# Optimization experiments

Measured on AMD Instinct MI355X. Metric: run time of the kernel, lower is better.

The kernel has to match this reference:

```python
import jax, jax.numpy as jnp
import numpy as np

B, L, D_IN, H, FEAT, PROJ = 1024, 128, 130, 768, 49, 40


def setup_inputs() -> dict:
    key = jax.random.key(0)
    ks = jax.random.split(key, 16)
    s = 0.05
    return {
        "X": jax.random.normal(ks[0], (B, L, D_IN), dtype=jnp.float32),
        "Fe": jax.random.normal(ks[1], (B, FEAT), dtype=jnp.float32),
        # three attention heads densa1/2/3 stacked: [3, H, L]
        "W_att": jax.random.normal(ks[2], (3, H, L), dtype=jnp.float32) * s,
        "b_att": jax.random.normal(ks[3], (3, L), dtype=jnp.float32) * s,
        # LSTMCell(3*D_IN, H) params, PyTorch layout
        "W_ih": jax.random.normal(ks[4], (4 * H, 3 * D_IN), dtype=jnp.float32) * s,
        "W_hh": jax.random.normal(ks[5], (4 * H, H), dtype=jnp.float32) * s,
        "b_ih": jax.random.normal(ks[6], (4 * H,), dtype=jnp.float32) * s,
        "b_hh": jax.random.normal(ks[7], (4 * H,), dtype=jnp.float32) * s,
        # Dense1: Linear(H, FEAT)
        "W_d1": jax.random.normal(ks[8], (FEAT, H), dtype=jnp.float32) * s,
        "b_d1": jax.random.normal(ks[9], (FEAT,), dtype=jnp.float32) * s,
        # AttFeat R: Linear(FEAT, PROJ); A: Linear(PROJ, 1, bias=False)
        "W_r": jax.random.normal(ks[10], (PROJ, FEAT), dtype=jnp.float32) * s,
        "b_r": jax.random.normal(ks[11], (PROJ,), dtype=jnp.float32) * s,
        "W_a": jax.random.normal(ks[12], (1, PROJ), dtype=jnp.float32) * s,
        # Dense2: Linear(PROJ, 2)
        "W_d2": jax.random.normal(ks[13], (2, PROJ), dtype=jnp.float32) * s,
        "b_d2": jax.random.normal(ks[14], (2,), dtype=jnp.float32) * s,
    }


def reference(X, Fe, W_att, b_att, W_ih, W_hh, b_ih, b_hh, W_d1, b_d1, W_r, b_r, W_a, W_d2, b_d2):
    b = X.shape[0]

    def step(carry, _):
        h, c = carry
        # three softmax attention distributions over the sequence: [b, 3, L]
        logits = jnp.einsum('bh,khl->bkl', h, W_att) + b_att
        alp = jax.nn.softmax(logits, axis=-1)
        # weighted sums over seq -> concat of v1,v2,v3: [b, 3*D_IN]
        v = jnp.einsum('bkl,bld->bkd', alp, X).reshape(b, -1)
        # PyTorch LSTMCell update
        gates = v @ W_ih.T + b_ih + h @ W_hh.T + b_hh
        i, f, g, o = jnp.split(gates, 4, axis=-1)
        c_new = jax.nn.sigmoid(f) * c + jax.nn.sigmoid(i) * jnp.tanh(g)
        h_new = jax.nn.sigmoid(o) * jnp.tanh(c_new)
        return (h_new, c_new), h_new

    h0 = jnp.zeros((b, H), dtype=X.dtype)
    c0 = jnp.zeros((b, H), dtype=X.dtype)
    _, hs = jax.lax.scan(step, (h0, c0), None, length=L)  # [L, b, H]
    out = jnp.transpose(hs, (1, 0, 2))                    # [b, L, H]

    # MaxLayer: max-pool over the sequence dim
    x = jnp.max(out, axis=1)                              # [b, H]

    # Dense1 + ReLU
    y = jax.nn.relu(x @ W_d1.T + b_d1)                    # [b, FEAT]

    # AttFeat over [y, Fe]
    r1 = jax.nn.leaky_relu(y @ W_r.T + b_r)               # [b, PROJ]
    r2 = jax.nn.leaky_relu(Fe @ W_r.T + b_r)
    a1 = jnp.tanh(r1) @ W_a.T                             # [b, 1]
    a2 = jnp.tanh(r2) @ W_a.T
    a = jax.nn.softmax(jnp.concatenate([a1, a2], axis=-1), axis=-1)  # [b, 2]
    s = jax.nn.relu(a[:, 0:1] * r1 + a[:, 1:2] * r2)      # [b, PROJ]

    # Dense2 (squeeze is a no-op for b > 1)
    return s @ W_d2.T + b_d2                              # [b, 2]
```

## Files before the change

kernel.cpp:

```cpp
#include <hip/hip_runtime.h>
#include <stdint.h>


#define B_SZ   1024
#define LSEQ   128
#define DIN    130
#define HDIM   768
#define NFEAT  49
#define NPROJ  40
#define KPAD   1216
#define VOFF   416
#define NGATE  3072
#define KT_G   19
#define XELEM  (LSEQ * DIN)
#define GBUF   20480

typedef unsigned short u16;
typedef __attribute__((ext_vector_type(8))) short short8;
typedef __attribute__((ext_vector_type(4))) float f32x4;

__device__ __forceinline__ u16 f2bf(float f) {
  unsigned int u = __float_as_uint(f);
  u += 0x7FFFu + ((u >> 16) & 1u);
  return (u16)(u >> 16);
}
__device__ __forceinline__ float bf2f(u16 b) {
  return __uint_as_float(((unsigned int)b) << 16);
}
__device__ __forceinline__ float frcp(float x) {
  return __builtin_amdgcn_rcpf(x);
}
__device__ __forceinline__ float ftanh(float x) {
  return 1.f - 2.f * frcp(1.f + __expf(2.f * x));
}
__device__ __forceinline__ float fsigm(float x) {
  return frcp(1.f + __expf(-x));
}
__device__ __forceinline__ void gload16(const void* g, void* l) {
  __builtin_amdgcn_global_load_lds(
      (__attribute__((address_space(1))) const void*)g,
      (__attribute__((address_space(3))) void*)l, 16, 0, 0);
}

__global__ __launch_bounds__(256, 4) void gemm_logits_k(
    const u16* __restrict__ Ah,
    const u16* __restrict__ Bh, float* __restrict__ Cp)
{
  __shared__ __align__(16) u16 sAh[32 * 40];
  __shared__ __align__(16) u16 sBh[64 * 40];

  const int tid = threadIdx.x, lane = tid & 63, wid = tid >> 6;
  const int wm = (wid & 1) * 16, wn = (wid >> 1) * 32;
  const int lm = lane & 15, quad = lane >> 4;
  const int bm = blockIdx.x * 32, bn = blockIdx.y * 64;
  const int kh = blockIdx.z;
  const int kbase = kh * 384;
  float* __restrict__ C = Cp + (size_t)kh * B_SZ * 384;

  const bool aload = tid < 128;
  const int ar = tid >> 2, ac = (tid & 3) * 8;
  const size_t a_off = (size_t)(bm + ar) * KPAD + kbase + ac;
  const size_t b_off = (size_t)(bn + ar) * HDIM + kbase + ac;

  uint4 ph, pb;
  if (aload) ph = *(const uint4*)(Ah + a_off);
  pb = *(const uint4*)(Bh + b_off);

  f32x4 acc0 = {0.f, 0.f, 0.f, 0.f}, acc1 = {0.f, 0.f, 0.f, 0.f};

  for (int kt = 0; kt < 12; ++kt) {
    if (aload) *(uint4*)&sAh[ar * 40 + ac] = ph;
    *(uint4*)&sBh[ar * 40 + ac] = pb;
    __syncthreads();
    if (kt + 1 < 12) {
      const int k0 = (kt + 1) * 32;
      if (aload) ph = *(const uint4*)(Ah + a_off + k0);
      pb = *(const uint4*)(Bh + b_off + k0);
    }
    const short8 ah = *(const short8*)&sAh[(wm + lm) * 40 + quad * 8];
    const short8 b0 = *(const short8*)&sBh[(wn + lm) * 40 + quad * 8];
    const short8 b1 = *(const short8*)&sBh[(wn + 16 + lm) * 40 + quad * 8];
    acc0 = __builtin_amdgcn_mfma_f32_16x16x32_bf16(ah, b0, acc0, 0, 0, 0);
    acc1 = __builtin_amdgcn_mfma_f32_16x16x32_bf16(ah, b1, acc1, 0, 0, 0);
    __syncthreads();
  }

  const int col = bn + wn + lm;
  const int row0 = bm + wm + quad * 4;
#pragma unroll
  for (int r = 0; r < 4; ++r) {
    C[(size_t)(row0 + r) * 384 + col]      = acc0[r];
    C[(size_t)(row0 + r) * 384 + col + 16] = acc1[r];
  }
}

__global__ __launch_bounds__(256, 2) void gates_lstm(
    const u16* __restrict__ Ah,
    const u16* __restrict__ Wh,
    const float* __restrict__ bsum,
    float* __restrict__ cst, float* __restrict__ hmax,
    u16* __restrict__ out_h)
{
  __shared__ __align__(16) char smem[2 * GBUF];

  const int tid = threadIdx.x, lane = tid & 63, wid = tid >> 6;
  const int wm = (wid >> 1) * 32, wn = (wid & 1) * 48;
  const int lm = lane & 15, quad = lane >> 4;

  const int wg = blockIdx.x;
  const int vid = (wg & 7) * 64 + (wg >> 3);
  const int bm = (vid & 15) * 64;
  const int j0 = (vid >> 4) * 24;

  const u16* Asrc[2];
#pragma unroll
  for (int i = 0; i < 2; ++i) {
    const int r = i * 32 + wid * 8 + (lane >> 3);
    const int s = (lane & 7) ^ (r & 7);
    Asrc[i] = Ah + (size_t)(bm + r) * KPAD + (s << 3);
  }
  const u16* Bsrc[3];
#pragma unroll
  for (int i = 0; i < 3; ++i) {
    const int r = i * 32 + wid * 8 + (lane >> 3);
    const int s = (lane & 7) ^ (r & 7);
    const int nrow = (r / 24) * HDIM + j0 + (r % 24);
    Bsrc[i] = Wh + (size_t)nrow * KPAD + (s << 3);
  }

  int aoff[2], boff[3];
#pragma unroll
  for (int mi = 0; mi < 2; ++mi) {
    const int R = wm + mi * 16 + lm;
    aoff[mi] = R * 64 + ((quad ^ (R & 7)) << 3);
  }
#pragma unroll
  for (int ni = 0; ni < 3; ++ni) {
    const int R = wn + ni * 16 + lm;
    boff[ni] = R * 64 + ((quad ^ (R & 7)) << 3);
  }

  f32x4 acc[2][3];
#pragma unroll
  for (int mi = 0; mi < 2; ++mi)
#pragma unroll
    for (int ni = 0; ni < 3; ++ni) acc[mi][ni] = (f32x4){0.f, 0.f, 0.f, 0.f};

  auto stage = [&](int buf, int kt) {
    char* bb = smem + buf * GBUF;
    const int k0 = kt * 64;
#pragma unroll
    for (int i = 0; i < 2; ++i)
      gload16(Asrc[i] + k0, bb + ((i << 12) + (wid << 10)));
#pragma unroll
    for (int i = 0; i < 3; ++i)
      gload16(Bsrc[i] + k0, bb + 8192 + ((i << 12) + (wid << 10)));
  };

  stage(0, 0);
  __syncthreads();

  for (int kt = 0; kt < KT_G; ++kt) {
    if (kt + 1 < KT_G) stage((kt + 1) & 1, kt + 1);
    const u16* sA = (const u16*)(smem + (kt & 1) * GBUF);
    const u16* sB = sA + 4096;
#pragma unroll
    for (int kk = 0; kk < 2; ++kk) {
      const int kx = kk << 5;
      short8 af[2], bg[3];
#pragma unroll
      for (int mi = 0; mi < 2; ++mi)
        af[mi] = *(const short8*)(sA + (aoff[mi] ^ kx));
#pragma unroll
      for (int ni = 0; ni < 3; ++ni)
        bg[ni] = *(const short8*)(sB + (boff[ni] ^ kx));
#pragma unroll
      for (int mi = 0; mi < 2; ++mi)
#pragma unroll
        for (int ni = 0; ni < 3; ++ni)
          acc[mi][ni] = __builtin_amdgcn_mfma_f32_16x16x32_bf16(
              af[mi], bg[ni], acc[mi][ni], 0, 0, 0);
    }
    __syncthreads();
  }

  float* tile = (float*)smem;
#pragma unroll
  for (int mi = 0; mi < 2; ++mi)
#pragma unroll
    for (int ni = 0; ni < 3; ++ni) {
      const int c = wn + ni * 16 + lm;
#pragma unroll
      for (int r = 0; r < 4; ++r)
        tile[(wm + mi * 16 + quad * 4 + r) * 100 + c] = acc[mi][ni][r];
    }
  __syncthreads();

#pragma unroll
  for (int i = 0; i < 6; ++i) {
    const int lin = tid + 256 * i;
    const int row = lin / 24, jj = lin - row * 24;
    const int b = bm + row, j = j0 + jj;
    const float* tr = tile + row * 100;
    const float pi = tr[jj]      + bsum[j];
    const float pf = tr[24 + jj] + bsum[HDIM + j];
    const float pg = tr[48 + jj] + bsum[2 * HDIM + j];
    const float po = tr[72 + jj] + bsum[3 * HDIM + j];
    const float si = fsigm(pi);
    const float sf = fsigm(pf);
    const float so = fsigm(po);
    const size_t cidx = (size_t)b * HDIM + j;
    const float cn = sf * cst[cidx] + si * ftanh(pg);
    const float hn = so * ftanh(cn);
    cst[cidx] = cn;
    hmax[cidx] = fmaxf(hmax[cidx], hn);
    out_h[(size_t)b * KPAD + VOFF + j] = f2bf(hn);
  }
}

__global__ __launch_bounds__(512, 4) void softmax_v(
    const float* __restrict__ l0, const float* __restrict__ l1,
    const float* __restrict__ b_att,
    const u16* __restrict__ XT,
    u16* __restrict__ act)
{
  const int b = blockIdx.x;
  const int t = threadIdx.x;
  __shared__ __align__(16) u16 sXT[XELEM];
  __shared__ __align__(16) float s_alp[384];
  __shared__ float s_w[16];

  {
    const uint4* src = (const uint4*)(XT + (size_t)b * XELEM);
    uint4* dst = (uint4*)sXT;
#pragma unroll
    for (int rep = 0; rep < 4; ++rep) {
      const int i = t + rep * 512;
      const int d = i >> 4, blk = i & 15;
      dst[d * 16 + (blk ^ (d & 7))] = src[i];
    }
    if (t < 32) {
      const int i = 2048 + t;
      const int d = i >> 4, blk = i & 15;
      dst[d * 16 + (blk ^ (d & 7))] = src[i];
    }
  }

  const int lane = t & 63, wv = t >> 6, hw = wv & ~1;
  float x = -3.4e38f;
  if (t < 384)
    x = l0[(size_t)b * 384 + t] + l1[(size_t)b * 384 + t] + b_att[t];

  float m = x;
#pragma unroll
  for (int off = 32; off > 0; off >>= 1) m = fmaxf(m, __shfl_xor(m, off));
  if (lane == 0 && wv < 6) s_w[wv] = m;
  __syncthreads();

  float e = 0.f;
  if (t < 384) e = __expf(x - fmaxf(s_w[hw], s_w[hw | 1]));
  float sum = e;
#pragma unroll
  for (int off = 32; off > 0; off >>= 1) sum += __shfl_xor(sum, off);
  if (lane == 0 && wv < 6) s_w[8 + wv] = sum;
  __syncthreads();

  if (t < 384) {
    const float sk = s_w[8 + hw] + s_w[8 + (hw | 1)];
    s_alp[t] = e * frcp(sk);
  }
  __syncthreads();

  if (t < 390) {
    const int k = t / 130;
    const int d = t - k * 130;
    const uint4* xr = (const uint4*)sXT;
    const int dbase = d * 16, dsw = d & 7;
    const float* ab = s_alp + (k << 7);
    float acc = 0.f;
#pragma unroll
    for (int c = 0; c < 16; ++c) {
      const uint4 raw = xr[dbase + (c ^ dsw)];
      const float4 a0 = *(const float4*)(ab + (c << 3));
      const float4 a1 = *(const float4*)(ab + (c << 3) + 4);
      acc += a0.x * bf2f((u16)(raw.x & 0xffff));
      acc += a0.y * bf2f((u16)(raw.x >> 16));
      acc += a0.z * bf2f((u16)(raw.y & 0xffff));
      acc += a0.w * bf2f((u16)(raw.y >> 16));
      acc += a1.x * bf2f((u16)(raw.z & 0xffff));
      acc += a1.y * bf2f((u16)(raw.z >> 16));
      acc += a1.z * bf2f((u16)(raw.w & 0xffff));
      acc += a1.w * bf2f((u16)(raw.w >> 16));
    }
    act[(size_t)b * KPAD + t] = f2bf(acc);
  }
}

__global__ __launch_bounds__(64) void final_head(
    const float* __restrict__ hmax, const float* __restrict__ Fe,
    const float* __restrict__ W_d1, const float* __restrict__ b_d1,
    const float* __restrict__ W_r,  const float* __restrict__ b_r,
    const float* __restrict__ W_a,
    const float* __restrict__ W_d2, const float* __restrict__ b_d2,
    float* __restrict__ out)
{
  const int b = blockIdx.x;
  const int t = threadIdx.x;
  __shared__ float sx[HDIM];
  __shared__ float sy[NFEAT];
  __shared__ float sr1[NPROJ], sr2[NPROJ];
  __shared__ float sa[2];

  for (int i = t; i < HDIM; i += 64) sx[i] = hmax[(size_t)b * HDIM + i];
  __syncthreads();

  if (t < NFEAT) {
    float acc = b_d1[t];
    const float* w = W_d1 + (size_t)t * HDIM;
    for (int i = 0; i < HDIM; ++i) acc += sx[i] * w[i];
    sy[t] = fmaxf(acc, 0.f);
  }
  __syncthreads();

  if (t < NPROJ) {
    float a1 = b_r[t], a2 = b_r[t];
    const float* w  = W_r + (size_t)t * NFEAT;
    const float* fe = Fe + (size_t)b * NFEAT;
    for (int i = 0; i < NFEAT; ++i) { a1 += sy[i] * w[i]; a2 += fe[i] * w[i]; }
    sr1[t] = (a1 > 0.f) ? a1 : 0.01f * a1;
    sr2[t] = (a2 > 0.f) ? a2 : 0.01f * a2;
  }
  __syncthreads();

  if (t == 0) {
    float a1 = 0.f, a2 = 0.f;
    for (int p = 0; p < NPROJ; ++p) {
      a1 += tanhf(sr1[p]) * W_a[p];
      a2 += tanhf(sr2[p]) * W_a[p];
    }
    const float mx = fmaxf(a1, a2);
    const float e1 = expf(a1 - mx), e2 = expf(a2 - mx);
    sa[0] = e1 / (e1 + e2);
    sa[1] = e2 / (e1 + e2);
  }
  __syncthreads();

  if (t < 2) {
    float acc = b_d2[t];
    const float* w = W_d2 + (size_t)t * NPROJ;
    for (int p = 0; p < NPROJ; ++p) {
      float s = sa[0] * sr1[p] + sa[1] * sr2[p];
      s = fmaxf(s, 0.f);
      acc += s * w[p];
    }
    out[(size_t)b * 2 + t] = acc;
  }
}

__global__ __launch_bounds__(256) void pack_w(
    const float* __restrict__ W_ih, const float* __restrict__ W_hh,
    const float* __restrict__ b_ih, const float* __restrict__ b_hh,
    u16* __restrict__ hi, float* __restrict__ bsum)
{
  const int idx = blockIdx.x * 256 + threadIdx.x;
  if (idx >= NGATE * KPAD) return;
  const int n = idx / KPAD;
  const int k = idx - n * KPAD;
  float v = 0.f;
  if (k < 3 * DIN)                       v = W_ih[(size_t)n * (3 * DIN) + k];
  else if (k >= VOFF && k < VOFF + HDIM) v = W_hh[(size_t)n * HDIM + (k - VOFF)];
  hi[idx] = f2bf(v);
  if (k == 0) bsum[n] = b_ih[n] + b_hh[n];
}

__global__ __launch_bounds__(256) void pack_watt(
    const float* __restrict__ W_att,
    u16* __restrict__ hi)
{
  const int idx = blockIdx.x * 256 + threadIdx.x;
  if (idx >= 384 * HDIM) return;
  const int n = idx / HDIM;
  const int h = idx - n * HDIM;
  const int katt = n >> 7;
  const int l = n & 127;
  hi[idx] = f2bf(W_att[((size_t)katt * HDIM + h) * LSEQ + l]);
}

__global__ __launch_bounds__(256) void pack_xt(
    const float* __restrict__ X, u16* __restrict__ XT)
{
  const int b = blockIdx.x;
  const int t = threadIdx.x;
  __shared__ u16 sX[XELEM];
  const float* src = X + (size_t)b * XELEM;
  for (int i = t; i < XELEM; i += 256) sX[i] = f2bf(src[i]);
  __syncthreads();
  uint4* dst = (uint4*)(XT + (size_t)b * XELEM);
  for (int u = t; u < 2080; u += 256) {
    const int d = u >> 4, blk = u & 15;
    const int lb = blk * 8;
    ushort4 w0, w1;
    w0.x = sX[(lb + 0) * DIN + d]; w0.y = sX[(lb + 1) * DIN + d];
    w0.z = sX[(lb + 2) * DIN + d]; w0.w = sX[(lb + 3) * DIN + d];
    w1.x = sX[(lb + 4) * DIN + d]; w1.y = sX[(lb + 5) * DIN + d];
    w1.z = sX[(lb + 6) * DIN + d]; w1.w = sX[(lb + 7) * DIN + d];
    uint4 o;
    o.x = (unsigned)w0.x | ((unsigned)w0.y << 16);
    o.y = (unsigned)w0.z | ((unsigned)w0.w << 16);
    o.z = (unsigned)w1.x | ((unsigned)w1.y << 16);
    o.w = (unsigned)w1.z | ((unsigned)w1.w << 16);
    dst[u] = o;
  }
}

__global__ __launch_bounds__(256) void init_state(
    u16* __restrict__ a0, u16* __restrict__ a1,
    float* __restrict__ cst, float* __restrict__ hmax)
{
  const int idx = blockIdx.x * 256 + threadIdx.x;
  if (idx < B_SZ * KPAD) { a0[idx] = 0; a1[idx] = 0; }
  if (idx < B_SZ * HDIM) { cst[idx] = 0.f; hmax[idx] = -3.4e38f; }
}

extern "C" void kernel_launch(void* const* d_in, const int* in_sizes, int n_in,
                              void* d_out, int out_size, void* d_ws, size_t ws_size,
                              hipStream_t stream) {
  const float* X     = (const float*)d_in[0];
  const float* Fe    = (const float*)d_in[1];
  const float* W_att = (const float*)d_in[2];
  const float* b_att = (const float*)d_in[3];
  const float* W_ih  = (const float*)d_in[4];
  const float* W_hh  = (const float*)d_in[5];
  const float* b_ih  = (const float*)d_in[6];
  const float* b_hh  = (const float*)d_in[7];
  const float* W_d1  = (const float*)d_in[8];
  const float* b_d1  = (const float*)d_in[9];
  const float* W_r   = (const float*)d_in[10];
  const float* b_r   = (const float*)d_in[11];
  const float* W_a   = (const float*)d_in[12];
  const float* W_d2  = (const float*)d_in[13];
  const float* b_d2  = (const float*)d_in[14];
  float* out = (float*)d_out;

  char* base = (char*)d_ws;
  size_t off = 0;
  auto alloc = [&](size_t nbytes) -> void* {
    void* p = base + off;
    off = (off + nbytes + 255) & ~(size_t)255;
    return p;
  };
  u16* act0    = (u16*)alloc((size_t)B_SZ * KPAD * 2);
  u16* act1    = (u16*)alloc((size_t)B_SZ * KPAD * 2);
  u16* wcat    = (u16*)alloc((size_t)NGATE * KPAD * 2);
  u16* watt    = (u16*)alloc((size_t)384 * HDIM * 2);
  u16* xt16    = (u16*)alloc((size_t)B_SZ * XELEM * 2);
  float* bsum  = (float*)alloc((size_t)NGATE * 4);
  float* lpart = (float*)alloc((size_t)2 * B_SZ * 384 * 4);
  float* cst   = (float*)alloc((size_t)B_SZ * HDIM * 4);
  float* hmax  = (float*)alloc((size_t)B_SZ * HDIM * 4);

  pack_w<<<(NGATE * KPAD + 255) / 256, 256, 0, stream>>>(W_ih, W_hh, b_ih, b_hh, wcat, bsum);
  pack_watt<<<(384 * HDIM + 255) / 256, 256, 0, stream>>>(W_att, watt);
  pack_xt<<<B_SZ, 256, 0, stream>>>(X, xt16);
  init_state<<<(B_SZ * KPAD + 255) / 256, 256, 0, stream>>>(act0, act1, cst, hmax);

  float* l0 = lpart;
  float* l1 = lpart + (size_t)B_SZ * 384;

  gemm_logits_k<<<dim3(B_SZ / 32, 384 / 64, 2), 256, 0, stream>>>(act0 + VOFF, watt, lpart);
  softmax_v<<<B_SZ, 512, 0, stream>>>(l0, l1, b_att, xt16, act0);

  u16 *rd = act0, *wr = act1;
  for (int step = 0; step < LSEQ; ++step) {
    gates_lstm<<<dim3(512), 256, 0, stream>>>(rd, wcat, bsum, cst, hmax, wr);
    if (step + 1 < LSEQ) {
      gemm_logits_k<<<dim3(B_SZ / 32, 384 / 64, 2), 256, 0, stream>>>(wr + VOFF, watt, lpart);
      softmax_v<<<B_SZ, 512, 0, stream>>>(l0, l1, b_att, xt16, wr);
    }
    u16* tt = rd; rd = wr; wr = tt;
  }

  final_head<<<B_SZ, 64, 0, stream>>>(hmax, Fe, W_d1, b_d1, W_r, b_r, W_a, W_d2, b_d2, out);
}
```

Measured before the change: 4.356 ms.

## Enlarge gates_lstm tile to 128x96 with 512 threads and split waitcnt

The LSTM gate GEMM now runs 256 workgroups of 512 threads, each computing a 128-row by 96-gate-column tile instead of 64 rows. This halves how often the weight tiles are reloaded across workgroups and gives one larger block per CU. The shared-memory stage buffer grows to hold the bigger A tile. The full __syncthreads is replaced by per-wave s_waitcnt vmcnt counts plus s_barrier, so the next stage's loads can stay in flight while the current tile is computed. The cost is fewer, larger blocks with less latency hiding between blocks, and correctness now depends on the hand-counted outstanding loads per wave.

```diff
diff --git a/kernel.cpp b/kernel.cpp
--- a/kernel.cpp
+++ b/kernel.cpp
@@ -13,7 +13,7 @@
 #define NGATE  3072
 #define KT_G   19
 #define XELEM  (LSEQ * DIN)
-#define GBUF   20480
+#define GBUF   28672
 
 typedef unsigned short u16;
 typedef __attribute__((ext_vector_type(8))) short short8;
@@ -94,7 +94,7 @@
   }
 }
 
-__global__ __launch_bounds__(256, 2) void gates_lstm(
+__global__ __launch_bounds__(512, 2) void gates_lstm(
     const u16* __restrict__ Ah,
     const u16* __restrict__ Wh,
     const float* __restrict__ bsum,
@@ -108,24 +108,29 @@
   const int lm = lane & 15, quad = lane >> 4;
 
   const int wg = blockIdx.x;
-  const int vid = (wg & 7) * 64 + (wg >> 3);
-  const int bm = (vid & 15) * 64;
-  const int j0 = (vid >> 4) * 24;
+  const int vid = (wg & 7) * 32 + (wg >> 3);
+  const int bm = (vid & 7) * 128;
+  const int j0 = (vid >> 3) * 24;
 
   const u16* Asrc[2];
 #pragma unroll
   for (int i = 0; i < 2; ++i) {
-    const int r = i * 32 + wid * 8 + (lane >> 3);
-    const int s = (lane & 7) ^ (r & 7);
+    const int r = i * 64 + (tid >> 3);
+    const int s = (tid & 7) ^ (r & 7);
     Asrc[i] = Ah + (size_t)(bm + r) * KPAD + (s << 3);
   }
-  const u16* Bsrc[3];
-#pragma unroll
-  for (int i = 0; i < 3; ++i) {
-    const int r = i * 32 + wid * 8 + (lane >> 3);
-    const int s = (lane & 7) ^ (r & 7);
-    const int nrow = (r / 24) * HDIM + j0 + (r % 24);
-    Bsrc[i] = Wh + (size_t)nrow * KPAD + (s << 3);
+  const u16* Bsrc0;
+  const u16* Bsrc1;
+  {
+    const int r0 = tid >> 3;
+    const int s0 = (tid & 7) ^ (r0 & 7);
+    const int nrow0 = (r0 / 24) * HDIM + j0 + (r0 % 24);
+    Bsrc0 = Wh + (size_t)nrow0 * KPAD + (s0 << 3);
+    const int r1 = 64 + (tid >> 3);
+    const int s1 = (tid & 7) ^ (r1 & 7);
+    const int r1c = (r1 < 96) ? r1 : 95;
+    const int nrow1 = (r1c / 24) * HDIM + j0 + (r1c % 24);
+    Bsrc1 = Wh + (size_t)nrow1 * KPAD + (s1 << 3);
   }
 
   int aoff[2], boff[3];
@@ -149,21 +154,27 @@
   auto stage = [&](int buf, int kt) {
     char* bb = smem + buf * GBUF;
     const int k0 = kt * 64;
-#pragma unroll
-    for (int i = 0; i < 2; ++i)
-      gload16(Asrc[i] + k0, bb + ((i << 12) + (wid << 10)));
-#pragma unroll
-    for (int i = 0; i < 3; ++i)
-      gload16(Bsrc[i] + k0, bb + 8192 + ((i << 12) + (wid << 10)));
+    gload16(Asrc[0] + k0, bb + (tid << 4));
+    gload16(Asrc[1] + k0, bb + 8192 + (tid << 4));
+    gload16(Bsrc0 + k0, bb + 16384 + (tid << 4));
+    if (tid < 256)
+      gload16(Bsrc1 + k0, bb + 24576 + (tid << 4));
   };
 
   stage(0, 0);
-  __syncthreads();
 
   for (int kt = 0; kt < KT_G; ++kt) {
-    if (kt + 1 < KT_G) stage((kt + 1) & 1, kt + 1);
+    if (kt + 1 < KT_G) {
+      stage((kt + 1) & 1, kt + 1);
+      if (wid < 4) asm volatile("s_waitcnt vmcnt(4)" ::: "memory");
+      else         asm volatile("s_waitcnt vmcnt(3)" ::: "memory");
+    } else {
+      asm volatile("s_waitcnt vmcnt(0)" ::: "memory");
+    }
+    asm volatile("s_barrier" ::: "memory");
+
     const u16* sA = (const u16*)(smem + (kt & 1) * GBUF);
-    const u16* sB = sA + 4096;
+    const u16* sB = sA + 8192;
 #pragma unroll
     for (int kk = 0; kk < 2; ++kk) {
       const int kx = kk << 5;
@@ -181,7 +192,7 @@
           acc[mi][ni] = __builtin_amdgcn_mfma_f32_16x16x32_bf16(
               af[mi], bg[ni], acc[mi][ni], 0, 0, 0);
     }
-    __syncthreads();
+    asm volatile("s_barrier" ::: "memory");
   }
 
   float* tile = (float*)smem;
@@ -198,7 +209,7 @@
 
 #pragma unroll
   for (int i = 0; i < 6; ++i) {
-    const int lin = tid + 256 * i;
+    const int lin = tid + 512 * i;
     const int row = lin / 24, jj = lin - row * 24;
     const int b = bm + row, j = j0 + jj;
     const float* tr = tile + row * 100;
@@ -472,7 +483,7 @@
 
   u16 *rd = act0, *wr = act1;
   for (int step = 0; step < LSEQ; ++step) {
-    gates_lstm<<<dim3(512), 256, 0, stream>>>(rd, wcat, bsum, cst, hmax, wr);
+    gates_lstm<<<dim3(256), 512, 0, stream>>>(rd, wcat, bsum, cst, hmax, wr);
     if (step + 1 < LSEQ) {
       gemm_logits_k<<<dim3(B_SZ / 32, 384 / 64, 2), 256, 0, stream>>>(wr + VOFF, watt, lpart);
       softmax_v<<<B_SZ, 512, 0, stream>>>(l0, l1, b_att, xt16, wr);
```

New measurement: 4.089 ms. 1.07x faster.
